# Kernel tuning notes

Measured on AMD Instinct MI355X. Metric: run time of the kernel, lower is better.

Reference implementation:

```python
import jax, jax.numpy as jnp
import numpy as np

ITERATIONS = 3
EPS = 1e-06

def squash(s):
    # square_norm along last dim, keepdims (matches torch squash)
    sq = jnp.sum(s * s, axis=-1, keepdims=True)
    return sq / (1.0 + sq) * s / (jnp.sqrt(sq) + EPS)

def setup_inputs() -> dict:
    key = jax.random.key(0)
    k1, k2 = jax.random.split(key)
    x = jax.random.normal(k1, (64, 32, 8, 8, 16), dtype=jnp.float32)
    W = jax.random.normal(k2, (1, 32, 8, 8, 32, 16, 32), dtype=jnp.float32)
    return {"x": x, "W": W}

def reference(x, W):
    # u_hat: (B, C, H, Wd, O, D) = x (B,C,H,Wd,I) @ W (C,H,Wd,O,I,D)
    u_hat = jnp.einsum('bchwi,chwoid->bchwod', x, W[0])
    b = jnp.zeros(u_hat.shape[:-1], dtype=u_hat.dtype)  # (B,C,H,Wd,O)
    for _ in range(ITERATIONS - 1):
        c = jax.nn.softmax(b, axis=-1)
        s = jnp.sum(c[..., None] * u_hat, axis=(1, 2, 3))  # (B,O,D)
        v = squash(s)
        b = b + jnp.sum(u_hat * v[:, None, None, None], axis=-1)
    c = jax.nn.softmax(b, axis=-1)
    s = jnp.sum(c[..., None] * u_hat, axis=(1, 2, 3))
    return squash(s)  # (B, out_capsules, out_cap_dim)
```

## Files before the change

kernel.cpp:

```cpp
#include <hip/hip_runtime.h>
#include <math.h>

#define B_ 64
#define N_ 2048
#define O_ 32
#define I_ 16
#define D_ 32
#define OD_ 1024

typedef __attribute__((ext_vector_type(8))) short bf16x8;
typedef __attribute__((ext_vector_type(4))) float f32x4;

union FragU { unsigned u[4]; uint4 v; bf16x8 f; };

__device__ __forceinline__ void barrier_lds() {
  asm volatile("s_waitcnt lgkmcnt(0)\n\ts_barrier" ::: "memory");
}

template <int CTRL>
__device__ __forceinline__ float dpp_mov_f(float x) {
  return __int_as_float(
      __builtin_amdgcn_update_dpp(0, __float_as_int(x), CTRL, 0xf, 0xf, true));
}
__device__ __forceinline__ float grp32_max(float x) {
  x = fmaxf(x, dpp_mov_f<0xb1>(x));
  x = fmaxf(x, dpp_mov_f<0x4e>(x));
  x = fmaxf(x, dpp_mov_f<0x124>(x));
  x = fmaxf(x, dpp_mov_f<0x128>(x));
  x = fmaxf(x, __shfl_xor(x, 16));
  return x;
}
__device__ __forceinline__ float grp32_sum(float x) {
  x += dpp_mov_f<0xb1>(x);
  x += dpp_mov_f<0x4e>(x);
  x += dpp_mov_f<0x124>(x);
  x += dpp_mov_f<0x128>(x);
  x += __shfl_xor(x, 16);
  return x;
}

__device__ __forceinline__ void dk_split(float f, unsigned &h, unsigned &l) {
  unsigned u = __float_as_uint(f);
  h = u & 0xffff0000u;
  float lo = f - __uint_as_float(h);
  l = __float_as_uint(lo) >> 16;
}
__device__ __forceinline__ void dk_split16(float f, unsigned short &h,
                                           unsigned short &l) {
  unsigned u = __float_as_uint(f);
  unsigned hu = u & 0xffff0000u;
  h = (unsigned short)(u >> 16);
  float lo = f - __uint_as_float(hu);
  l = (unsigned short)(__float_as_uint(lo) >> 16);
}
__device__ __forceinline__ unsigned pk(unsigned short e0, unsigned short e1) {
  return (unsigned)e0 | ((unsigned)e1 << 16);
}

__global__ __launch_bounds__(256) void prep_all(const float* __restrict__ W,
                                                const float* __restrict__ x,
                                                uint4* __restrict__ WP,
                                                uint4* __restrict__ XP) {
  __shared__ float tile[8 * 512];
  const int tid = threadIdx.x;
  if (blockIdx.x < 8192) {
    const int pair0 = blockIdx.x * 8;
    const f32x4* gsrc = (const f32x4*)(W + (size_t)pair0 * 512);
    f32x4* lds4 = (f32x4*)tile;
#pragma unroll
    for (int k = 0; k < 4; ++k)
      lds4[tid + k * 256] = __builtin_nontemporal_load(gsrc + tid + k * 256);
    __syncthreads();
    const int p = tid >> 5;
    const int d = tid & 31;
    const int pair = pair0 + p;
    unsigned short hh[I_], ll[I_];
#pragma unroll
    for (int i = 0; i < I_; ++i)
      dk_split16(tile[p * 512 + i * 32 + d], hh[i], ll[i]);
    const int c = d & 15, dhalf = d >> 4;
    size_t base = ((size_t)pair * 2 + dhalf) * 4;
#pragma unroll
    for (int sel = 0; sel < 2; ++sel) {
      const unsigned short* e = sel ? ll : hh;
#pragma unroll
      for (int qp = 0; qp < 2; ++qp) {
        uint4 u;
        u.x = pk(e[qp * 8 + 0], e[qp * 8 + 1]);
        u.y = pk(e[qp * 8 + 2], e[qp * 8 + 3]);
        u.z = pk(e[qp * 8 + 4], e[qp * 8 + 5]);
        u.w = pk(e[qp * 8 + 6], e[qp * 8 + 7]);
        WP[(base + sel * 2 + qp) * 16 + c] = u;
      }
    }
  } else {
    int t = (blockIdx.x - 8192) * 256 + tid;
    int c = t & 15, n = (t >> 4) & 2047, bg = t >> 15;
    const f32x4* xq = (const f32x4*)(x + ((size_t)(bg * 16 + c) * N_ + n) * I_);
    float xv[I_];
#pragma unroll
    for (int k = 0; k < 4; ++k) {
      f32x4 q4 = __builtin_nontemporal_load(xq + k);
      xv[4 * k + 0] = q4[0];
      xv[4 * k + 1] = q4[1];
      xv[4 * k + 2] = q4[2];
      xv[4 * k + 3] = q4[3];
    }
    unsigned short hh[I_], ll[I_];
#pragma unroll
    for (int i = 0; i < I_; ++i) dk_split16(xv[i], hh[i], ll[i]);
    size_t base = ((size_t)bg * N_ + n) * 4;
#pragma unroll
    for (int sel = 0; sel < 2; ++sel) {
      const unsigned short* e = sel ? ll : hh;
#pragma unroll
      for (int qp = 0; qp < 2; ++qp) {
        uint4 u;
        u.x = pk(e[qp * 8 + 0], e[qp * 8 + 1]);
        u.y = pk(e[qp * 8 + 2], e[qp * 8 + 3]);
        u.z = pk(e[qp * 8 + 4], e[qp * 8 + 5]);
        u.w = pk(e[qp * 8 + 6], e[qp * 8 + 7]);
        XP[(base + sel * 2 + qp) * 16 + c] = u;
      }
    }
  }
}

template <int UNIFORM>
__global__ __launch_bounds__(1024, 4) void mfma_pass6(
    const uint4* __restrict__ XP, const uint4* __restrict__ WP,
    const float* __restrict__ v, float* __restrict__ partial, int NC) {
  const int tid = threadIdx.x;
  const int lane = tid & 63;
  const int w = tid >> 6;
  const int q = lane >> 4;
  const int c = lane & 15;
  const int qp = q & 1;
  const int ch = blockIdx.x;
  const int bgy = blockIdx.y;

  __shared__ uint4 xps[2][16][4][16];
  __shared__ float ls_l[32 * 33];
  __shared__ float ls_c2[32 * 33];

  const int n0 = ch * NC;

  {
    uint4* xf = (uint4*)xps;
    const int total = 2 * NC * 64;
    for (int l = tid; l < total; l += 1024) {
      int bgl = l / (NC * 64);
      int rest = l - bgl * (NC * 64);
      xf[bgl * 1024 + rest] =
          XP[(size_t)(bgy * 2 + bgl) * 131072 + (size_t)n0 * 64 + rest];
    }
  }

  f32x4 s_t[2][4];
#pragma unroll
  for (int bgl = 0; bgl < 2; ++bgl)
#pragma unroll
    for (int ct = 0; ct < 4; ++ct) s_t[bgl][ct] = (f32x4){0.f, 0.f, 0.f, 0.f};

  float vreg[2][4][4];
  if (!UNIFORM) {
#pragma unroll
    for (int bgl = 0; bgl < 2; ++bgl)
#pragma unroll
      for (int ct = 0; ct < 4; ++ct) {
        const float4 vv = *(const float4*)&v[(size_t)(bgy * 32 + bgl * 16 + c) * OD_ +
                                             (2 * w + (ct >> 1)) * 32 +
                                             (ct & 1) * 16 + q * 4];
        vreg[bgl][ct][0] = vv.x;
        vreg[bgl][ct][1] = vv.y;
        vreg[bgl][ct][2] = vv.z;
        vreg[bgl][ct][3] = vv.w;
      }
  }

  barrier_lds();

  const uint4* wbase = WP + (size_t)(2 * w) * 128 + lane;

  FragU cb[4];
#pragma unroll
  for (int ct = 0; ct < 4; ++ct)
    cb[ct].v = wbase[(size_t)n0 * 4096 + ct * 64];

  if (UNIFORM) {
    for (int nl = 0; nl < NC; ++nl) {
      const size_t n = (size_t)(n0 + nl);
      const size_t np = (nl + 1 < NC) ? n + 1 : n;
      FragU cbn[4];
#pragma unroll
      for (int ct = 0; ct < 4; ++ct) cbn[ct].v = wbase[np * 4096 + ct * 64];
#pragma unroll
      for (int bgl = 0; bgl < 2; ++bgl) {
        FragU ah, al;
        ah.v = xps[bgl][nl][qp][c];
        al.v = xps[bgl][nl][2 + qp][c];
#pragma unroll
        for (int ct = 0; ct < 4; ++ct) {
          s_t[bgl][ct] = __builtin_amdgcn_mfma_f32_16x16x32_bf16(
              ah.f, cb[ct].f, s_t[bgl][ct], 0, 0, 0);
          s_t[bgl][ct] = __builtin_amdgcn_mfma_f32_16x16x32_bf16(
              al.f, cb[ct].f, s_t[bgl][ct], 0, 0, 0);
        }
      }
#pragma unroll
      for (int ct = 0; ct < 4; ++ct) cb[ct] = cbn[ct];
    }
  } else {
    for (int nl = 0; nl < NC; ++nl) {
      const size_t n = (size_t)(n0 + nl);
      const size_t np = (nl + 1 < NC) ? n + 1 : n;

#pragma unroll
      for (int bgl = 0; bgl < 2; ++bgl) {
        FragU ah, al;
        ah.v = xps[bgl][nl][qp][c];
        al.v = xps[bgl][nl][2 + qp][c];
        float lgol[2] = {0.f, 0.f};
#pragma unroll
        for (int ct = 0; ct < 4; ++ct) {
          f32x4 accT = (f32x4){0.f, 0.f, 0.f, 0.f};
          accT = __builtin_amdgcn_mfma_f32_16x16x32_bf16(cb[ct].f, ah.f, accT, 0, 0, 0);
          f32x4 uT = __builtin_amdgcn_mfma_f32_16x16x32_bf16(cb[ct].f, al.f, accT, 0, 0, 0);
          const int ol = ct >> 1;
#pragma unroll
          for (int r = 0; r < 4; ++r)
            lgol[ol] = fmaf(uT[r], vreg[bgl][ct][r], lgol[ol]);
        }
#pragma unroll
        for (int ol = 0; ol < 2; ++ol) {
          float t = lgol[ol];
          t += __shfl_xor(t, 16);
          t += __shfl_xor(t, 32);
          if (q == 0) ls_l[(2 * w + ol) * 33 + bgl * 16 + c] = t;
        }
      }
      FragU cbn[4];
#pragma unroll
      for (int ct = 0; ct < 4; ++ct) cbn[ct].v = wbase[np * 4096 + ct * 64];

      barrier_lds();
      {
        const int idx = (tid & 31) * 33 + (tid >> 5);
        float l = ls_l[idx];
        float mx = grp32_max(l);
        float e = __expf(l - mx);
        float sm = grp32_sum(e);
        ls_c2[idx] = e / sm;
      }
      barrier_lds();
#pragma unroll
      for (int bgl = 0; bgl < 2; ++bgl) {
        FragU ah, al;
        ah.v = xps[bgl][nl][qp][c];
        al.v = xps[bgl][nl][2 + qp][c];
#pragma unroll
        for (int ct = 0; ct < 4; ++ct) {
          f32x4 acc = (f32x4){0.f, 0.f, 0.f, 0.f};
          acc = __builtin_amdgcn_mfma_f32_16x16x32_bf16(ah.f, cb[ct].f, acc, 0, 0, 0);
          f32x4 u = __builtin_amdgcn_mfma_f32_16x16x32_bf16(al.f, cb[ct].f, acc, 0, 0, 0);
          const int o = 2 * w + (ct >> 1);
#pragma unroll
          for (int r = 0; r < 4; ++r) {
            float cc = ls_c2[o * 33 + bgl * 16 + q * 4 + r];
            s_t[bgl][ct][r] = fmaf(cc, u[r], s_t[bgl][ct][r]);
          }
        }
      }
#pragma unroll
      for (int ct = 0; ct < 4; ++ct) cb[ct] = cbn[ct];
    }
  }

  const float scale = UNIFORM ? (1.f / 32.f) : 1.f;
#pragma unroll
  for (int bgl = 0; bgl < 2; ++bgl)
#pragma unroll
    for (int ct = 0; ct < 4; ++ct) {
      int odc = (2 * w + (ct >> 1)) * 32 + (ct & 1) * 16 + c;
#pragma unroll
      for (int r = 0; r < 4; ++r) {
        partial[((size_t)ch * B_ + bgy * 32 + bgl * 16 + q * 4 + r) * OD_ + odc] =
            s_t[bgl][ct][r] * scale;
      }
    }
}

template <int UNIFORM>
__global__ __launch_bounds__(512, 4) void mfma_pass_fb(
    const float* __restrict__ x, const float* __restrict__ W,
    const float* __restrict__ v, float* __restrict__ partial, int NC) {
  const int tid = threadIdx.x;
  const int lane = tid & 63;
  const int cg = tid >> 6;
  const int q = lane >> 4;
  const int c = lane & 15;
  const int ch = blockIdx.x;
  const int bg = blockIdx.y;

  __shared__ float ls_logit[16 * O_];
  __shared__ float ls_c[16 * O_];

  f32x4 s_t[8];
#pragma unroll
  for (int ct = 0; ct < 8; ++ct) s_t[ct] = (f32x4){0.f, 0.f, 0.f, 0.f};

  const int n0 = ch * NC;
  const int ih = (q & 1) * 8;
  const float* xrow = x + ((size_t)(bg * 16 + c) * N_) * I_ + ih;

  for (int nl = 0; nl < NC; ++nl) {
    const int n = n0 + nl;
    const float* xp = xrow + (size_t)n * I_;
    float4 xv0 = *(const float4*)xp;
    float4 xv1 = *(const float4*)(xp + 4);
    float xv[8] = {xv0.x, xv0.y, xv0.z, xv0.w, xv1.x, xv1.y, xv1.z, xv1.w};
    FragU a1;
#pragma unroll
    for (int p = 0; p < 4; ++p) {
      unsigned h0, l0, h1, l1;
      dk_split(xv[2 * p], h0, l0);
      dk_split(xv[2 * p + 1], h1, l1);
      a1.u[p] = (q < 2) ? ((h0 >> 16) | h1) : (l0 | (l1 << 16));
    }
    f32x4 u_t[8];
#pragma unroll
    for (int ct = 0; ct < 8; ++ct) {
      const int o = cg * 4 + (ct >> 1);
      const int d = (ct & 1) * 16 + c;
      const float* wp = W + (((size_t)n * O_ + o) * I_ + ih) * D_ + d;
      FragU b1, b2;
#pragma unroll
      for (int p = 0; p < 4; ++p) {
        unsigned h0, l0, h1, l1;
        dk_split(wp[(2 * p) * D_], h0, l0);
        dk_split(wp[(2 * p + 1) * D_], h1, l1);
        b1.u[p] = (h0 >> 16) | h1;
        b2.u[p] = l0 | (l1 << 16);
      }
      if (UNIFORM) {
        s_t[ct] = __builtin_amdgcn_mfma_f32_16x16x32_bf16(a1.f, b1.f, s_t[ct], 0, 0, 0);
        s_t[ct] = __builtin_amdgcn_mfma_f32_16x16x32_bf16(a1.f, b2.f, s_t[ct], 0, 0, 0);
      } else {
        f32x4 acc = (f32x4){0.f, 0.f, 0.f, 0.f};
        acc = __builtin_amdgcn_mfma_f32_16x16x32_bf16(a1.f, b1.f, acc, 0, 0, 0);
        u_t[ct] = __builtin_amdgcn_mfma_f32_16x16x32_bf16(a1.f, b2.f, acc, 0, 0, 0);
      }
    }
    if (!UNIFORM) {
#pragma unroll
      for (int ol = 0; ol < 4; ++ol) {
        float lg[4] = {0.f, 0.f, 0.f, 0.f};
#pragma unroll
        for (int hf = 0; hf < 2; ++hf) {
          int ct = ol * 2 + hf;
          int odc = cg * 128 + ct * 16 + c;
#pragma unroll
          for (int r = 0; r < 4; ++r)
            lg[r] = fmaf(u_t[ct][r], v[(size_t)(bg * 16 + q * 4 + r) * OD_ + odc], lg[r]);
        }
#pragma unroll
        for (int r = 0; r < 4; ++r) {
#pragma unroll
          for (int m = 1; m < 16; m <<= 1) lg[r] += __shfl_xor(lg[r], m);
        }
        if (c == 0) {
#pragma unroll
          for (int r = 0; r < 4; ++r)
            ls_logit[(q * 4 + r) * O_ + cg * 4 + ol] = lg[r];
        }
      }
      __syncthreads();
      {
        int b_l = tid >> 5, o = tid & 31;
        float l = ls_logit[b_l * O_ + o];
        float mx = l;
#pragma unroll
        for (int m = 16; m >= 1; m >>= 1) mx = fmaxf(mx, __shfl_xor(mx, m));
        float e = __expf(l - mx);
        float sm = e;
#pragma unroll
        for (int m = 16; m >= 1; m >>= 1) sm += __shfl_xor(sm, m);
        ls_c[b_l * O_ + o] = e / sm;
      }
      __syncthreads();
#pragma unroll
      for (int ol = 0; ol < 4; ++ol) {
        int o = cg * 4 + ol;
        float cc[4];
#pragma unroll
        for (int r = 0; r < 4; ++r) cc[r] = ls_c[(q * 4 + r) * O_ + o];
#pragma unroll
        for (int hf = 0; hf < 2; ++hf) {
          int ct = ol * 2 + hf;
#pragma unroll
          for (int r = 0; r < 4; ++r)
            s_t[ct][r] = fmaf(cc[r], u_t[ct][r], s_t[ct][r]);
        }
      }
    }
  }

  const float scale = UNIFORM ? (1.f / 32.f) : 1.f;
#pragma unroll
  for (int ct = 0; ct < 8; ++ct) {
#pragma unroll
    for (int r = 0; r < 4; ++r) {
      partial[((size_t)ch * B_ + bg * 16 + q * 4 + r) * OD_ + cg * 128 + ct * 16 + c] =
          s_t[ct][r] * scale;
    }
  }
}

__global__ __launch_bounds__(256) void reduce_fused(
    const float4* __restrict__ part, int cq4, const float4* __restrict__ prev,
    float4* __restrict__ out) {
  __shared__ float4 accs[4][64];
  const int lane = threadIdx.x & 63;
  const int cg = threadIdx.x >> 6;
  const int g4 = blockIdx.x * 64 + lane;
  float4 s = make_float4(0.f, 0.f, 0.f, 0.f);
  const int c0 = cg * cq4;
  for (int i = 0; i < cq4; ++i) {
    float4 p = part[(size_t)(c0 + i) * 16384 + g4];
    s.x += p.x; s.y += p.y; s.z += p.z; s.w += p.w;
  }
  accs[cg][lane] = s;
  __syncthreads();
  if (cg == 0) {
    float4 a1 = accs[1][lane], a2 = accs[2][lane], a3 = accs[3][lane];
    s.x += a1.x + a2.x + a3.x;
    s.y += a1.y + a2.y + a3.y;
    s.z += a1.z + a2.z + a3.z;
    s.w += a1.w + a2.w + a3.w;
    float sq = s.x * s.x + s.y * s.y + s.z * s.z + s.w * s.w;
#pragma unroll
    for (int m = 4; m >= 1; m >>= 1) sq += __shfl_xor(sq, m, 8);
    float scale = sq / ((1.f + sq) * (sqrtf(sq) + 1e-6f));
    float4 r = make_float4(s.x * scale, s.y * scale, s.z * scale, s.w * scale);
    if (prev) {
      float4 p = prev[g4];
      r.x += p.x; r.y += p.y; r.z += p.z; r.w += p.w;
    }
    out[g4] = r;
  }
}

__global__ __launch_bounds__(256) void reduce_squash(
    const float4* __restrict__ part, int chunks,
    const float4* __restrict__ prev, float4* __restrict__ out) {
  int g4 = blockIdx.x * 256 + threadIdx.x;
  float4 s = make_float4(0.f, 0.f, 0.f, 0.f);
#pragma unroll 4
  for (int ch = 0; ch < chunks; ++ch) {
    float4 p = part[(size_t)ch * 16384 + g4];
    s.x += p.x; s.y += p.y; s.z += p.z; s.w += p.w;
  }
  float sq = s.x * s.x + s.y * s.y + s.z * s.z + s.w * s.w;
#pragma unroll
  for (int m = 4; m >= 1; m >>= 1) sq += __shfl_xor(sq, m, 8);
  float scale = sq / ((1.f + sq) * (sqrtf(sq) + 1e-6f));
  float4 r = make_float4(s.x * scale, s.y * scale, s.z * scale, s.w * scale);
  if (prev) {
    float4 p = prev[g4];
    r.x += p.x; r.y += p.y; r.z += p.z; r.w += p.w;
  }
  out[g4] = r;
}

extern "C" void kernel_launch(void* const* d_in, const int* in_sizes, int n_in,
                              void* d_out, int out_size, void* d_ws,
                              size_t ws_size, hipStream_t stream) {
  const float* x = (const float*)d_in[0];
  const float* W = (const float*)d_in[1];
  float* out = (float*)d_out;

  const size_t XP_FLOATS = 4ull * 2048 * 4 * 16 * 4;
  const size_t WP_FLOATS = 2048ull * 32 * 2 * 4 * 16 * 4;

  float* v1 = (float*)d_ws;
  float* vsum = v1 + 65536;
  float* partial = vsum + 65536;

  const int chunks = 128;
  bool packed_path =
      (131072 + (size_t)chunks * 65536 + XP_FLOATS + WP_FLOATS) * 4 <= ws_size;

  if (packed_path) {
    uint4* XP = (uint4*)(partial + (size_t)chunks * 65536);
    uint4* WP = XP + XP_FLOATS / 4;
    const int NC = N_ / chunks;
    const int cq4 = chunks / 4;
    dim3 grid(chunks, 2);

    prep_all<<<8704, 256, 0, stream>>>(W, x, WP, XP);

    mfma_pass6<1><<<grid, 1024, 0, stream>>>(XP, WP, nullptr, partial, NC);
    reduce_fused<<<256, 256, 0, stream>>>((const float4*)partial, cq4, nullptr,
                                          (float4*)v1);
    mfma_pass6<0><<<grid, 1024, 0, stream>>>(XP, WP, v1, partial, NC);
    reduce_fused<<<256, 256, 0, stream>>>((const float4*)partial, cq4,
                                          (const float4*)v1, (float4*)vsum);
    mfma_pass6<0><<<grid, 1024, 0, stream>>>(XP, WP, vsum, partial, NC);
    reduce_fused<<<256, 256, 0, stream>>>((const float4*)partial, cq4, nullptr,
                                          (float4*)out);
  } else {
    int fchunks = 128;
    while (fchunks > 1 && (131072 + (size_t)fchunks * 65536) * 4 > ws_size)
      fchunks >>= 1;
    int NC = N_ / fchunks;
    dim3 grid(fchunks, 4);

    mfma_pass_fb<1><<<grid, 512, 0, stream>>>(x, W, nullptr, partial, NC);
    reduce_squash<<<64, 256, 0, stream>>>((const float4*)partial, fchunks,
                                          nullptr, (float4*)v1);
    mfma_pass_fb<0><<<grid, 512, 0, stream>>>(x, W, v1, partial, NC);
    reduce_squash<<<64, 256, 0, stream>>>((const float4*)partial, fchunks,
                                          (const float4*)v1, (float4*)vsum);
    mfma_pass_fb<0><<<grid, 512, 0, stream>>>(x, W, vsum, partial, NC);
    reduce_squash<<<64, 256, 0, stream>>>((const float4*)partial, fchunks,
                                          nullptr, (float4*)out);
  }
}
```

Baseline: 348.1 us.

## Fuse W bf16 hi/lo packing into the first routing pass

The W-packing half of the prep kernel is removed. The first MFMA pass (uniform coupling) now streams raw fp32 W through per-wave LDS staging with register prefetch of the next n, splits each value into bf16 hi/lo fragments on the fly, and uses them directly. Blocks with bgy==0 also write the packed WP fragments for the later passes. This drops one full read of the large packed-W tensor between prep and pass 1. In exchange the split arithmetic is repeated for both bgy blocks, W is read once per bgy, and the kernel needs much more LDS per block.

Result: slower. 359.4 us (+3.2%).

```diff
diff --git a/kernel.cpp b/kernel.cpp
--- a/kernel.cpp
+++ b/kernel.cpp
@@ -57,73 +57,151 @@
   return (unsigned)e0 | ((unsigned)e1 << 16);
 }
 
-__global__ __launch_bounds__(256) void prep_all(const float* __restrict__ W,
-                                                const float* __restrict__ x,
-                                                uint4* __restrict__ WP,
-                                                uint4* __restrict__ XP) {
-  __shared__ float tile[8 * 512];
+__global__ __launch_bounds__(256) void prep_x(const float* __restrict__ x,
+                                              uint4* __restrict__ XP) {
   const int tid = threadIdx.x;
-  if (blockIdx.x < 8192) {
-    const int pair0 = blockIdx.x * 8;
-    const f32x4* gsrc = (const f32x4*)(W + (size_t)pair0 * 512);
-    f32x4* lds4 = (f32x4*)tile;
-#pragma unroll
-    for (int k = 0; k < 4; ++k)
-      lds4[tid + k * 256] = __builtin_nontemporal_load(gsrc + tid + k * 256);
-    __syncthreads();
-    const int p = tid >> 5;
-    const int d = tid & 31;
-    const int pair = pair0 + p;
-    unsigned short hh[I_], ll[I_];
-#pragma unroll
-    for (int i = 0; i < I_; ++i)
-      dk_split16(tile[p * 512 + i * 32 + d], hh[i], ll[i]);
-    const int c = d & 15, dhalf = d >> 4;
-    size_t base = ((size_t)pair * 2 + dhalf) * 4;
-#pragma unroll
-    for (int sel = 0; sel < 2; ++sel) {
-      const unsigned short* e = sel ? ll : hh;
-#pragma unroll
-      for (int qp = 0; qp < 2; ++qp) {
-        uint4 u;
-        u.x = pk(e[qp * 8 + 0], e[qp * 8 + 1]);
-        u.y = pk(e[qp * 8 + 2], e[qp * 8 + 3]);
-        u.z = pk(e[qp * 8 + 4], e[qp * 8 + 5]);
-        u.w = pk(e[qp * 8 + 6], e[qp * 8 + 7]);
-        WP[(base + sel * 2 + qp) * 16 + c] = u;
-      }
-    }
-  } else {
-    int t = (blockIdx.x - 8192) * 256 + tid;
-    int c = t & 15, n = (t >> 4) & 2047, bg = t >> 15;
-    const f32x4* xq = (const f32x4*)(x + ((size_t)(bg * 16 + c) * N_ + n) * I_);
-    float xv[I_];
-#pragma unroll
-    for (int k = 0; k < 4; ++k) {
-      f32x4 q4 = __builtin_nontemporal_load(xq + k);
-      xv[4 * k + 0] = q4[0];
-      xv[4 * k + 1] = q4[1];
-      xv[4 * k + 2] = q4[2];
-      xv[4 * k + 3] = q4[3];
-    }
-    unsigned short hh[I_], ll[I_];
-#pragma unroll
-    for (int i = 0; i < I_; ++i) dk_split16(xv[i], hh[i], ll[i]);
-    size_t base = ((size_t)bg * N_ + n) * 4;
-#pragma unroll
-    for (int sel = 0; sel < 2; ++sel) {
-      const unsigned short* e = sel ? ll : hh;
-#pragma unroll
-      for (int qp = 0; qp < 2; ++qp) {
-        uint4 u;
-        u.x = pk(e[qp * 8 + 0], e[qp * 8 + 1]);
-        u.y = pk(e[qp * 8 + 2], e[qp * 8 + 3]);
-        u.z = pk(e[qp * 8 + 4], e[qp * 8 + 5]);
-        u.w = pk(e[qp * 8 + 6], e[qp * 8 + 7]);
-        XP[(base + sel * 2 + qp) * 16 + c] = u;
-      }
-    }
-  }
+  int t = blockIdx.x * 256 + tid;
+  int c = t & 15, n = (t >> 4) & 2047, bg = t >> 15;
+  const f32x4* xq = (const f32x4*)(x + ((size_t)(bg * 16 + c) * N_ + n) * I_);
+  float xv[I_];
+#pragma unroll
+  for (int k = 0; k < 4; ++k) {
+    f32x4 q4 = __builtin_nontemporal_load(xq + k);
+    xv[4 * k + 0] = q4[0];
+    xv[4 * k + 1] = q4[1];
+    xv[4 * k + 2] = q4[2];
+    xv[4 * k + 3] = q4[3];
+  }
+  unsigned short hh[I_], ll[I_];
+#pragma unroll
+  for (int i = 0; i < I_; ++i) dk_split16(xv[i], hh[i], ll[i]);
+  size_t base = ((size_t)bg * N_ + n) * 4;
+#pragma unroll
+  for (int sel = 0; sel < 2; ++sel) {
+    const unsigned short* e = sel ? ll : hh;
+#pragma unroll
+    for (int qp = 0; qp < 2; ++qp) {
+      uint4 u;
+      u.x = pk(e[qp * 8 + 0], e[qp * 8 + 1]);
+      u.y = pk(e[qp * 8 + 2], e[qp * 8 + 3]);
+      u.z = pk(e[qp * 8 + 4], e[qp * 8 + 5]);
+      u.w = pk(e[qp * 8 + 6], e[qp * 8 + 7]);
+      XP[(base + sel * 2 + qp) * 16 + c] = u;
+    }
+  }
+}
+
+__global__ __launch_bounds__(1024, 4) void pass1_fused(
+    const uint4* __restrict__ XP, const float* __restrict__ W,
+    uint4* __restrict__ WP, float* __restrict__ partial, int NC) {
+  const int tid = threadIdx.x;
+  const int lane = tid & 63;
+  const int w = tid >> 6;
+  const int q = lane >> 4;
+  const int c = lane & 15;
+  const int qp = q & 1;
+  const int ch = blockIdx.x;
+  const int bgy = blockIdx.y;
+
+  __shared__ uint4 xps[2][16][4][16];
+  __shared__ float wstage[16][1024];
+
+  const int n0 = ch * NC;
+
+  {
+    uint4* xf = (uint4*)xps;
+    const int total = 2 * NC * 64;
+    for (int l = tid; l < total; l += 1024) {
+      int bgl = l / (NC * 64);
+      int rest = l - bgl * (NC * 64);
+      xf[bgl * 1024 + rest] =
+          XP[(size_t)(bgy * 2 + bgl) * 131072 + (size_t)n0 * 64 + rest];
+    }
+  }
+
+  f32x4 s_t[2][4];
+#pragma unroll
+  for (int bgl = 0; bgl < 2; ++bgl)
+#pragma unroll
+    for (int ct = 0; ct < 4; ++ct) s_t[bgl][ct] = (f32x4){0.f, 0.f, 0.f, 0.f};
+
+  const float* wsrc = W + (size_t)(2 * w) * 512;
+  f32x4* ws4 = (f32x4*)wstage[w];
+  const float* ws = wstage[w];
+
+  f32x4 wreg[4];
+  {
+    const f32x4* g = (const f32x4*)(wsrc + (size_t)n0 * 16384);
+#pragma unroll
+    for (int k = 0; k < 4; ++k) wreg[k] = g[lane + k * 64];
+#pragma unroll
+    for (int k = 0; k < 4; ++k) ws4[lane + k * 64] = wreg[k];
+  }
+
+  barrier_lds();
+
+  for (int nl = 0; nl < NC; ++nl) {
+    const size_t n = (size_t)(n0 + nl);
+    const size_t np = (nl + 1 < NC) ? n + 1 : n;
+    {
+      const f32x4* g = (const f32x4*)(wsrc + np * 16384);
+#pragma unroll
+      for (int k = 0; k < 4; ++k) wreg[k] = g[lane + k * 64];
+    }
+    FragU cb[4];
+#pragma unroll
+    for (int ct = 0; ct < 4; ++ct) {
+      const int ol = ct >> 1, dh = ct & 1;
+      const float* base = ws + ol * 512 + qp * 256 + dh * 16 + c;
+      unsigned short e8[8];
+#pragma unroll
+      for (int e = 0; e < 8; ++e) {
+        float f = base[e * 32];
+        unsigned u = __float_as_uint(f);
+        unsigned short hi = (unsigned short)(u >> 16);
+        unsigned short lo = (unsigned short)(
+            __float_as_uint(f - __uint_as_float(u & 0xffff0000u)) >> 16);
+        e8[e] = (q < 2) ? hi : lo;
+      }
+      cb[ct].u[0] = pk(e8[0], e8[1]);
+      cb[ct].u[1] = pk(e8[2], e8[3]);
+      cb[ct].u[2] = pk(e8[4], e8[5]);
+      cb[ct].u[3] = pk(e8[6], e8[7]);
+    }
+    if (bgy == 0) {
+      uint4* wpdst = WP + n * 4096 + (size_t)(2 * w) * 128 + lane;
+#pragma unroll
+      for (int ct = 0; ct < 4; ++ct) wpdst[ct * 64] = cb[ct].v;
+    }
+#pragma unroll
+    for (int bgl = 0; bgl < 2; ++bgl) {
+      FragU ah, al;
+      ah.v = xps[bgl][nl][qp][c];
+      al.v = xps[bgl][nl][2 + qp][c];
+#pragma unroll
+      for (int ct = 0; ct < 4; ++ct) {
+        s_t[bgl][ct] = __builtin_amdgcn_mfma_f32_16x16x32_bf16(
+            ah.f, cb[ct].f, s_t[bgl][ct], 0, 0, 0);
+        s_t[bgl][ct] = __builtin_amdgcn_mfma_f32_16x16x32_bf16(
+            al.f, cb[ct].f, s_t[bgl][ct], 0, 0, 0);
+      }
+    }
+#pragma unroll
+    for (int k = 0; k < 4; ++k) ws4[lane + k * 64] = wreg[k];
+  }
+
+  const float scale = 1.f / 32.f;
+#pragma unroll
+  for (int bgl = 0; bgl < 2; ++bgl)
+#pragma unroll
+    for (int ct = 0; ct < 4; ++ct) {
+      int odc = (2 * w + (ct >> 1)) * 32 + (ct & 1) * 16 + c;
+#pragma unroll
+      for (int r = 0; r < 4; ++r) {
+        partial[((size_t)ch * B_ + bgy * 32 + bgl * 16 + q * 4 + r) * OD_ + odc] =
+            s_t[bgl][ct][r] * scale;
+      }
+    }
 }
 
 template <int UNIFORM>
@@ -497,9 +575,9 @@
     const int cq4 = chunks / 4;
     dim3 grid(chunks, 2);
 
-    prep_all<<<8704, 256, 0, stream>>>(W, x, WP, XP);
-
-    mfma_pass6<1><<<grid, 1024, 0, stream>>>(XP, WP, nullptr, partial, NC);
+    prep_x<<<512, 256, 0, stream>>>(x, XP);
+
+    pass1_fused<<<grid, 1024, 0, stream>>>(XP, W, WP, partial, NC);
     reduce_fused<<<256, 256, 0, stream>>>((const float4*)partial, cq4, nullptr,
                                           (float4*)v1);
     mfma_pass6<0><<<grid, 1024, 0, stream>>>(XP, WP, v1, partial, NC);
```
